# Performance work log

Measured on AMD Instinct MI355X. Metric: run time of the kernel, lower is better.

Reference implementation:

```python
import math
import jax, jax.numpy as jnp
import numpy as np

B, N, M, H = 2, 4096, 32, 8
FDIM, LDIM, HID = 256, 10, 16
D = FDIM // H  # head_dim = 32


def setup_inputs() -> dict:
    key = jax.random.key(0)
    ks = jax.random.split(key, 16)
    rn = lambda i, shape, scale=1.0: jax.random.normal(ks[i], shape, jnp.float32) * scale
    return {
        "nbhd_pairwise_g": rn(0, (B, N, M, LDIM)),
        "nbhd_mask": jax.random.bernoulli(ks[1], 0.9, (B, N, M)),
        "key_features": rn(2, (B, N, FDIM)),
        "query_features": rn(3, (B, N, FDIM)),
        "nbhd_idx": jax.random.randint(ks[4], (B, N, M), 0, N, dtype=jnp.int32),
        # fc_k / fc_q (Linear feature_dim -> embed_dim)
        "Wk": rn(5, (FDIM, FDIM), 1.0 / math.sqrt(FDIM)),
        "bk": rn(6, (FDIM,), 0.01),
        "Wq": rn(7, (FDIM, FDIM), 1.0 / math.sqrt(FDIM)),
        "bq": rn(8, (FDIM,), 0.01),
        "W0": rn(9, (H, LDIM, HID), 1.0 / math.sqrt(LDIM)),
        "b0": rn(10, (H, HID), 0.01),
        "W1": rn(11, (H, HID, HID), 1.0 / math.sqrt(HID)),
        "b1": rn(12, (H, HID), 0.01),
        "W2": rn(13, (H, HID, 1), 1.0 / math.sqrt(HID)),
        "b2": rn(14, (H, 1), 0.01),
    }


def reference(nbhd_pairwise_g, nbhd_mask, key_features, query_features, nbhd_idx,
              Wk, bk, Wq, bq, W0, b0, W1, b1, W2, b2):
    # --- DotProductKernel: project, gather keys at nbhd_idx, scaled dot ---
    K = (key_features @ Wk + bk).reshape(B, N, H, D)      # (b,n,h,d)
    Q = (query_features @ Wq + bq).reshape(B, N, H, D)    # (b,n,h,d)
    # gather neighbor keys: Kn[b,i,j] = K[b, nbhd_idx[b,i,j]]  -> (b,n,m,h,d)
    Kn = K[jnp.arange(B)[:, None, None], nbhd_idx]
    # same math as full QK^T followed by A_[B,NNS,nbhd_idx], without the n x n matrix
    feat = jnp.einsum('bnhd,bnmhd->bnmh', Q, Kn) / math.sqrt(D)  # (b,n,m,h)

    # --- location featurisation: per-head MLP on pairwise group embedding ---
    h0 = jax.nn.silu(jnp.einsum('bnml,hlk->bnmhk', nbhd_pairwise_g, W0) + b0)
    h1 = jax.nn.silu(jnp.einsum('bnmhk,hkj->bnmhj', h0, W1) + b1)
    loc = jax.nn.silu(jnp.einsum('bnmhj,hjo->bnmho', h1, W2) + b2)[..., 0]  # (b,n,m,h)

    # --- combination 'sum' (both unsqueezed to 5D), normalisation 'none' ---
    out = (feat + loc)[..., None]  # (b,n,m,h,1)
    return out
```

## Files before the change

kernel.cpp:

```cpp
#include <hip/hip_runtime.h>

typedef unsigned int   u32;
typedef unsigned short u16;
typedef __bf16 bf16x8 __attribute__((ext_vector_type(8)));
typedef float  f32x4  __attribute__((ext_vector_type(4)));
typedef float  f32x16 __attribute__((ext_vector_type(16)));

__device__ __forceinline__ u16 f2b(float f) {
  u32 u = __float_as_uint(f);
  u = (u + 0x7fffu + ((u >> 16) & 1u)) >> 16;
  return (u16)u;
}
__device__ __forceinline__ float silu_f(float x) { return __fdividef(x, 1.f + __expf(-x)); }

__global__ __launch_bounds__(512) void prep_all(
    const float* __restrict__ g,
    const float* __restrict__ Wk, const float* __restrict__ Wq,
    const float* __restrict__ W0, const float* __restrict__ W1,
    const float* __restrict__ b0, const float* __restrict__ b1,
    const float* __restrict__ W2,
    u16* __restrict__ Wkt, u16* __restrict__ Wqt,
    u16* __restrict__ W0A, u16* __restrict__ W1A,
    float* __restrict__ BT2, u16* __restrict__ G2, int useG2) {
  const int blk = blockIdx.x, t = threadIdx.x;
  if (blk < 1024) {
    if (!useG2) return;
    const int sub = t >> 6, lane = t & 63;
    const int hf = lane >> 5, m = lane & 31;
    const int bn = blk * 8 + sub;
    const float* gp = g + ((size_t)bn * 32 + m) * 10;
    bf16x8 gf = {};
    float2 v0 = *(const float2*)(gp + hf * 8);
    gf[0] = (__bf16)v0.x; gf[1] = (__bf16)v0.y;
    if (hf == 0) {
      float2 v1 = *(const float2*)(gp + 2);
      float2 v2 = *(const float2*)(gp + 4);
      float2 v3 = *(const float2*)(gp + 6);
      gf[2] = (__bf16)v1.x; gf[3] = (__bf16)v1.y;
      gf[4] = (__bf16)v2.x; gf[5] = (__bf16)v2.y;
      gf[6] = (__bf16)v3.x; gf[7] = (__bf16)v3.y;
    }
    *(bf16x8*)(G2 + ((size_t)bn * 64 + lane) * 8) = gf;
  } else if (blk < 1088) {
    for (int idx = (blk - 1024) * 512 + t; idx < 65536; idx += 64 * 512) {
      int n = idx >> 8, k = idx & 255;
      Wkt[idx] = f2b(Wk[k * 256 + n]);
      Wqt[idx] = f2b(Wq[k * 256 + n]);
    }
  } else {
    const int h = t >> 6, l = t & 63;
    const int hf = l >> 5, j = l & 31;
    float vals[24];
    #pragma unroll
    for (int e = 0; e < 8; e++) {
      int k = 8 * hf + e;
      float v0 = (j < 16 && k < 10) ? W0[h * 160 + k * 16 + j] : 0.f;
      W0A[t * 8 + e] = f2b(v0);
      int jin = (k & 3) + 8 * ((k >> 2) & 1) + 4 * (k >> 3);
      float v1 = (j < 16) ? W1[h * 256 + jin * 16 + j] : 0.f;
      W1A[t * 8 + e] = f2b(v1);
      int cj = (e & 3) + 8 * (e >> 2) + 4 * hf;
      vals[e]      = b0[h * 16 + cj];
      vals[8 + e]  = b1[h * 16 + cj];
      vals[16 + e] = W2[h * 16 + cj];
    }
    #pragma unroll
    for (int j4 = 0; j4 < 6; j4++)
      ((float4*)BT2)[j4 * 512 + t] =
        make_float4(vals[4 * j4], vals[4 * j4 + 1], vals[4 * j4 + 2], vals[4 * j4 + 3]);
  }
}

#define LDA 72
__global__ __launch_bounds__(256) void gemm_proj(
    const float* __restrict__ A0, const float* __restrict__ A1,
    const u16* __restrict__ B0, const u16* __restrict__ B1,
    const float* __restrict__ bias0, const float* __restrict__ bias1,
    u16* __restrict__ C0, u16* __restrict__ C1) {
  const float* A; const u16* Bt; const float* bias; u16* C;
  if (blockIdx.z == 0) { A = A0; Bt = B0; bias = bias0; C = C0; }
  else                 { A = A1; Bt = B1; bias = bias1; C = C1; }
  __shared__ __align__(16) u16 As[128 * LDA];
  __shared__ __align__(16) u16 Bs[128 * LDA];
  const int t = threadIdx.x;
  const int w = t >> 6, lane = t & 63;
  const int wm = w >> 1, wn = w & 1;
  const int row0 = blockIdx.x * 128, col0 = blockIdx.y * 128;
  f32x4 acc[4][4] = {};
  for (int kk = 0; kk < 256; kk += 64) {
    #pragma unroll
    for (int p = 0; p < 8; p++) {
      int r = p * 16 + (t >> 4), q = (t & 15) * 4;
      float4 v = *(const float4*)(A + (size_t)(row0 + r) * 256 + kk + q);
      uint2 pk;
      pk.x = (u32)f2b(v.x) | ((u32)f2b(v.y) << 16);
      pk.y = (u32)f2b(v.z) | ((u32)f2b(v.w) << 16);
      *(uint2*)(&As[r * LDA + q]) = pk;
    }
    #pragma unroll
    for (int p = 0; p < 4; p++) {
      int r = p * 32 + (t >> 3), q = (t & 7) * 8;
      *(uint4*)(&Bs[r * LDA + q]) = *(const uint4*)(Bt + (size_t)(col0 + r) * 256 + kk + q);
    }
    __syncthreads();
    #pragma unroll
    for (int ks = 0; ks < 2; ks++) {
      bf16x8 af[4], bfr[4];
      #pragma unroll
      for (int i = 0; i < 4; i++) {
        af[i]  = *(const bf16x8*)(&As[(wm * 64 + i * 16 + (lane & 15)) * LDA + ks * 32 + (lane >> 4) * 8]);
        bfr[i] = *(const bf16x8*)(&Bs[(wn * 64 + i * 16 + (lane & 15)) * LDA + ks * 32 + (lane >> 4) * 8]);
      }
      #pragma unroll
      for (int i = 0; i < 4; i++)
        #pragma unroll
        for (int j = 0; j < 4; j++)
          acc[i][j] = __builtin_amdgcn_mfma_f32_16x16x32_bf16(af[i], bfr[j], acc[i][j], 0, 0, 0);
    }
    __syncthreads();
  }
  #pragma unroll
  for (int j = 0; j < 4; j++) {
    int c = col0 + wn * 64 + j * 16 + (lane & 15);
    float bv = bias[c];
    #pragma unroll
    for (int i = 0; i < 4; i++) {
      int r0 = row0 + wm * 64 + i * 16 + (lane >> 4) * 4;
      #pragma unroll
      for (int q = 0; q < 4; q++)
        C[(size_t)(r0 + q) * 256 + c] = f2b(acc[i][j][q] + bv);
    }
  }
}

template<int USE_G2>
__global__ __launch_bounds__(512) void fused_main(
    const u16* __restrict__ Kbf, const u16* __restrict__ Qbf,
    const int* __restrict__ nidx, const float* __restrict__ g,
    const u16* __restrict__ W0A, const u16* __restrict__ W1A,
    const float* __restrict__ BT2, const float* __restrict__ b2,
    const u16* __restrict__ G2, float* __restrict__ out) {
  __shared__ float lout[256];
  const int t = threadIdx.x;
  const int h = t >> 6, lane = t & 63;
  const int hf = lane >> 5, m = lane & 31;
  const int bn = blockIdx.x;
  const int b = bn >> 12;
  const int row = bn * 32 + m;
  const int hs = __builtin_amdgcn_readfirstlane(h);

  const bf16x8 a0 = *(const bf16x8*)(W0A + (size_t)(hs * 64 + lane) * 8);
  const bf16x8 a1 = *(const bf16x8*)(W1A + (size_t)(hs * 64 + lane) * 8);
  const float4* bt = (const float4*)BT2;
  const float4 t0 = bt[0 * 512 + t], t1 = bt[1 * 512 + t], t2 = bt[2 * 512 + t];
  const float4 t3 = bt[3 * 512 + t], t4 = bt[4 * 512 + t], t5 = bt[5 * 512 + t];
  const float bj0[8] = {t0.x, t0.y, t0.z, t0.w, t1.x, t1.y, t1.z, t1.w};
  const float bj1[8] = {t2.x, t2.y, t2.z, t2.w, t3.x, t3.y, t3.z, t3.w};
  const float wj[8]  = {t4.x, t4.y, t4.z, t4.w, t5.x, t5.y, t5.z, t5.w};
  const float b2s = b2[hs];

  bf16x8 gf;
  if (USE_G2) {
    gf = *(const bf16x8*)(G2 + ((size_t)bn * 64 + lane) * 8);
  } else {
    bf16x8 gt = {};
    const float* gp = g + (size_t)row * 10;
    float2 v0 = *(const float2*)(gp + hf * 8);
    gt[0] = (__bf16)v0.x; gt[1] = (__bf16)v0.y;
    if (hf == 0) {
      float2 v1 = *(const float2*)(gp + 2);
      float2 v2 = *(const float2*)(gp + 4);
      float2 v3 = *(const float2*)(gp + 6);
      gt[2] = (__bf16)v1.x; gt[3] = (__bf16)v1.y;
      gt[4] = (__bf16)v2.x; gt[5] = (__bf16)v2.y;
      gt[6] = (__bf16)v3.x; gt[7] = (__bf16)v3.y;
    }
    gf = gt;
  }

  const int kidx = nidx[row];
  const u16* qbase = Qbf + ((size_t)bn << 8) + (hs << 5);
  const u16* kbase = Kbf + (((size_t)b << 12) + (size_t)kidx) * 256 + (hs << 5);
  const bf16x8 aq0 = *(const bf16x8*)(qbase + hf * 8);
  const bf16x8 aq1 = *(const bf16x8*)(qbase + 16 + hf * 8);
  const bf16x8 bk0 = *(const bf16x8*)(kbase + hf * 8);
  const bf16x8 bk1 = *(const bf16x8*)(kbase + 16 + hf * 8);

  const f32x16 z = {};
  f32x16 fa = __builtin_amdgcn_mfma_f32_32x32x16_bf16(aq0, bk0, z, 0, 0, 0);
  fa = __builtin_amdgcn_mfma_f32_32x32x16_bf16(aq1, bk1, fa, 0, 0, 0);
  const float feat = fa[0] * 0.17677669529663687f;

  f32x16 acc = __builtin_amdgcn_mfma_f32_32x32x16_bf16(a0, gf, z, 0, 0, 0);
  bf16x8 h0b;
  #pragma unroll
  for (int e = 0; e < 8; e++) h0b[e] = (__bf16)silu_f(acc[e] + bj0[e]);

  acc = __builtin_amdgcn_mfma_f32_32x32x16_bf16(a1, h0b, z, 0, 0, 0);
  float part = 0.f;
  #pragma unroll
  for (int e = 0; e < 8; e++) part += silu_f(acc[e] + bj1[e]) * wj[e];

  float osum = part + __shfl_xor(part, 32, 64);
  float res = feat + silu_f(osum + b2s);

  if (hf == 0) lout[m * 8 + h] = res;
  __syncthreads();
  if (t < 64) {
    float4 v = ((const float4*)lout)[t];
    ((float4*)(out + ((size_t)bn << 8)))[t] = v;
  }
}

extern "C" void kernel_launch(void* const* d_in, const int* in_sizes, int n_in,
                              void* d_out, int out_size, void* d_ws, size_t ws_size,
                              hipStream_t stream) {
  const float* g_in = (const float*)d_in[0];
  const float* kf   = (const float*)d_in[2];
  const float* qf   = (const float*)d_in[3];
  const int*   idx  = (const int*)d_in[4];
  const float* Wk   = (const float*)d_in[5];
  const float* bk   = (const float*)d_in[6];
  const float* Wq   = (const float*)d_in[7];
  const float* bq   = (const float*)d_in[8];
  const float* W0   = (const float*)d_in[9];
  const float* b0   = (const float*)d_in[10];
  const float* W1   = (const float*)d_in[11];
  const float* b1   = (const float*)d_in[12];
  const float* W2   = (const float*)d_in[13];
  const float* b2   = (const float*)d_in[14];

  char* ws = (char*)d_ws;
  u16*   Wkt = (u16*)(ws);
  u16*   Wqt = (u16*)(ws + 131072);
  u16*   W0A = (u16*)(ws + 262144);
  u16*   W1A = (u16*)(ws + 270336);
  float* BT2 = (float*)(ws + 278528);
  u16*   Kbf = (u16*)(ws + 524288);
  u16*   Qbf = (u16*)(ws + 524288 + 4194304);
  u16*   G2  = (u16*)(ws + 524288 + 8388608);

  const int useG2 = (ws_size >= (size_t)17408 * 1024) ? 1 : 0;

  prep_all<<<1089, 512, 0, stream>>>(g_in, Wk, Wq, W0, W1, b0, b1, W2,
                                     Wkt, Wqt, W0A, W1A, BT2, G2, useG2);
  gemm_proj<<<dim3(64, 2, 2), 256, 0, stream>>>(kf, qf, Wkt, Wqt, bk, bq, Kbf, Qbf);
  if (useG2)
    fused_main<1><<<8192, 512, 0, stream>>>(Kbf, Qbf, idx, g_in, W0A, W1A, BT2, b2,
                                            G2, (float*)d_out);
  else
    fused_main<0><<<8192, 512, 0, stream>>>(Kbf, Qbf, idx, g_in, W0A, W1A, BT2, b2,
                                            G2, (float*)d_out);
}
```

Before: 64.23 us.

## Split fused_main into two head-group blocks and fold query scale into Wq

```diff
diff --git a/kernel.cpp b/kernel.cpp
--- a/kernel.cpp
+++ b/kernel.cpp
@@ -12,6 +12,8 @@
   return (u16)u;
 }
 __device__ __forceinline__ float silu_f(float x) { return __fdividef(x, 1.f + __expf(-x)); }
+
+#define QSCALE 0.17677669529663687f
 
 __global__ __launch_bounds__(512) void prep_all(
     const float* __restrict__ g,
@@ -45,7 +47,7 @@
     for (int idx = (blk - 1024) * 512 + t; idx < 65536; idx += 64 * 512) {
       int n = idx >> 8, k = idx & 255;
       Wkt[idx] = f2b(Wk[k * 256 + n]);
-      Wqt[idx] = f2b(Wq[k * 256 + n]);
+      Wqt[idx] = f2b(Wq[k * 256 + n] * QSCALE);
     }
   } else {
     const int h = t >> 6, l = t & 63;
@@ -77,9 +79,9 @@
     const u16* __restrict__ B0, const u16* __restrict__ B1,
     const float* __restrict__ bias0, const float* __restrict__ bias1,
     u16* __restrict__ C0, u16* __restrict__ C1) {
-  const float* A; const u16* Bt; const float* bias; u16* C;
-  if (blockIdx.z == 0) { A = A0; Bt = B0; bias = bias0; C = C0; }
-  else                 { A = A1; Bt = B1; bias = bias1; C = C1; }
+  const float* A; const u16* Bt; const float* bias; u16* C; float bscale;
+  if (blockIdx.z == 0) { A = A0; Bt = B0; bias = bias0; C = C0; bscale = 1.f; }
+  else                 { A = A1; Bt = B1; bias = bias1; C = C1; bscale = QSCALE; }
   __shared__ __align__(16) u16 As[128 * LDA];
   __shared__ __align__(16) u16 Bs[128 * LDA];
   const int t = threadIdx.x;
@@ -122,7 +124,7 @@
   #pragma unroll
   for (int j = 0; j < 4; j++) {
     int c = col0 + wn * 64 + j * 16 + (lane & 15);
-    float bv = bias[c];
+    float bv = bias[c] * bscale;
     #pragma unroll
     for (int i = 0; i < 4; i++) {
       int r0 = row0 + wm * 64 + i * 16 + (lane >> 4) * 4;
@@ -134,26 +136,30 @@
 }
 
 template<int USE_G2>
-__global__ __launch_bounds__(512) void fused_main(
+__global__ __launch_bounds__(256) void fused_main(
     const u16* __restrict__ Kbf, const u16* __restrict__ Qbf,
     const int* __restrict__ nidx, const float* __restrict__ g,
     const u16* __restrict__ W0A, const u16* __restrict__ W1A,
     const float* __restrict__ BT2, const float* __restrict__ b2,
     const u16* __restrict__ G2, float* __restrict__ out) {
-  __shared__ float lout[256];
+  __shared__ float lout[128];
   const int t = threadIdx.x;
-  const int h = t >> 6, lane = t & 63;
+  const int lane = t & 63;
   const int hf = lane >> 5, m = lane & 31;
   const int bn = blockIdx.x;
+  const int hg = blockIdx.y;
   const int b = bn >> 12;
   const int row = bn * 32 + m;
-  const int hs = __builtin_amdgcn_readfirstlane(h);
-
-  const bf16x8 a0 = *(const bf16x8*)(W0A + (size_t)(hs * 64 + lane) * 8);
-  const bf16x8 a1 = *(const bf16x8*)(W1A + (size_t)(hs * 64 + lane) * 8);
+  const int hs = __builtin_amdgcn_readfirstlane(hg * 4 + (t >> 6));
+
+  const int kidx = nidx[row];
+
+  const int tt = hg * 256 + t;
+  const bf16x8 a0 = *(const bf16x8*)(W0A + (size_t)tt * 8);
+  const bf16x8 a1 = *(const bf16x8*)(W1A + (size_t)tt * 8);
   const float4* bt = (const float4*)BT2;
-  const float4 t0 = bt[0 * 512 + t], t1 = bt[1 * 512 + t], t2 = bt[2 * 512 + t];
-  const float4 t3 = bt[3 * 512 + t], t4 = bt[4 * 512 + t], t5 = bt[5 * 512 + t];
+  const float4 t0 = bt[0 * 512 + tt], t1 = bt[1 * 512 + tt], t2 = bt[2 * 512 + tt];
+  const float4 t3 = bt[3 * 512 + tt], t4 = bt[4 * 512 + tt], t5 = bt[5 * 512 + tt];
   const float bj0[8] = {t0.x, t0.y, t0.z, t0.w, t1.x, t1.y, t1.z, t1.w};
   const float bj1[8] = {t2.x, t2.y, t2.z, t2.w, t3.x, t3.y, t3.z, t3.w};
   const float wj[8]  = {t4.x, t4.y, t4.z, t4.w, t5.x, t5.y, t5.z, t5.w};
@@ -178,7 +184,6 @@
     gf = gt;
   }
 
-  const int kidx = nidx[row];
   const u16* qbase = Qbf + ((size_t)bn << 8) + (hs << 5);
   const u16* kbase = Kbf + (((size_t)b << 12) + (size_t)kidx) * 256 + (hs << 5);
   const bf16x8 aq0 = *(const bf16x8*)(qbase + hf * 8);
@@ -189,7 +194,7 @@
   const f32x16 z = {};
   f32x16 fa = __builtin_amdgcn_mfma_f32_32x32x16_bf16(aq0, bk0, z, 0, 0, 0);
   fa = __builtin_amdgcn_mfma_f32_32x32x16_bf16(aq1, bk1, fa, 0, 0, 0);
-  const float feat = fa[0] * 0.17677669529663687f;
+  const float feat = fa[0];
 
   f32x16 acc = __builtin_amdgcn_mfma_f32_32x32x16_bf16(a0, gf, z, 0, 0, 0);
   bf16x8 h0b;
@@ -197,18 +202,20 @@
   for (int e = 0; e < 8; e++) h0b[e] = (__bf16)silu_f(acc[e] + bj0[e]);
 
   acc = __builtin_amdgcn_mfma_f32_32x32x16_bf16(a1, h0b, z, 0, 0, 0);
-  float part = 0.f;
-  #pragma unroll
-  for (int e = 0; e < 8; e++) part += silu_f(acc[e] + bj1[e]) * wj[e];
+  float q0 = silu_f(acc[0] + bj1[0]) * wj[0] + silu_f(acc[1] + bj1[1]) * wj[1];
+  float q1 = silu_f(acc[2] + bj1[2]) * wj[2] + silu_f(acc[3] + bj1[3]) * wj[3];
+  float q2 = silu_f(acc[4] + bj1[4]) * wj[4] + silu_f(acc[5] + bj1[5]) * wj[5];
+  float q3 = silu_f(acc[6] + bj1[6]) * wj[6] + silu_f(acc[7] + bj1[7]) * wj[7];
+  float part = (q0 + q1) + (q2 + q3);
 
   float osum = part + __shfl_xor(part, 32, 64);
   float res = feat + silu_f(osum + b2s);
 
-  if (hf == 0) lout[m * 8 + h] = res;
+  if (hf == 0) lout[m * 4 + (t >> 6)] = res;
   __syncthreads();
-  if (t < 64) {
+  if (t < 32) {
     float4 v = ((const float4*)lout)[t];
-    ((float4*)(out + ((size_t)bn << 8)))[t] = v;
+    *(float4*)(out + ((size_t)bn << 8) + t * 8 + hg * 4) = v;
   }
 }
 
@@ -246,9 +253,9 @@
                                      Wkt, Wqt, W0A, W1A, BT2, G2, useG2);
   gemm_proj<<<dim3(64, 2, 2), 256, 0, stream>>>(kf, qf, Wkt, Wqt, bk, bq, Kbf, Qbf);
   if (useG2)
-    fused_main<1><<<8192, 512, 0, stream>>>(Kbf, Qbf, idx, g_in, W0A, W1A, BT2, b2,
-                                            G2, (float*)d_out);
+    fused_main<1><<<dim3(8192, 2), 256, 0, stream>>>(Kbf, Qbf, idx, g_in, W0A, W1A,
+                                                     BT2, b2, G2, (float*)d_out);
   else
-    fused_main<0><<<8192, 512, 0, stream>>>(Kbf, Qbf, idx, g_in, W0A, W1A, BT2, b2,
-                                            G2, (float*)d_out);
-}
+    fused_main<0><<<dim3(8192, 2), 256, 0, stream>>>(Kbf, Qbf, idx, g_in, W0A, W1A,
+                                                     BT2, b2, G2, (float*)d_out);
+}
```

Measured after the change: 69.26 us. 7.8% more time.
